# Kernel optimization log

Measured on AMD Instinct MI355X. Metric: run time of the kernel, lower is better.

The kernel has to match this reference:

```python
import jax, jax.numpy as jnp
import numpy as np

TOPK = 13
NUM_CLASSES = 80
ALPHA = 1.0
BETA = 6.0
EPS = 1e-9
DYN_T = 0.4


def _ciou(box1, box2, eps=1e-7):
    # box1, box2: broadcastable [..., 4] in xyxy; returns CIoU [...]
    b1x1, b1y1, b1x2, b1y2 = jnp.split(box1, 4, axis=-1)
    b2x1, b2y1, b2x2, b2y2 = jnp.split(box2, 4, axis=-1)
    w1, h1 = b1x2 - b1x1, b1y2 - b1y1
    w2, h2 = b2x2 - b2x1, b2y2 - b2y1
    inter = (jnp.minimum(b1x2, b2x2) - jnp.maximum(b1x1, b2x1)).clip(0) * \
            (jnp.minimum(b1y2, b2y2) - jnp.maximum(b1y1, b2y1)).clip(0)
    union = w1 * h1 + w2 * h2 - inter + eps
    iou = inter / union
    cw = jnp.maximum(b1x2, b2x2) - jnp.minimum(b1x1, b2x1)   # enclosing box w
    ch = jnp.maximum(b1y2, b2y2) - jnp.minimum(b1y1, b2y1)   # enclosing box h
    c2 = cw ** 2 + ch ** 2 + eps
    rho2 = ((b2x1 + b2x2 - b1x1 - b1x2) ** 2 + (b2y1 + b2y2 - b1y1 - b1y2) ** 2) / 4.0
    v = (4.0 / jnp.pi ** 2) * (jnp.arctan(w2 / h2) - jnp.arctan(w1 / h1)) ** 2
    a = jax.lax.stop_gradient(v / (v - iou + (1.0 + eps)))
    return (iou - (rho2 / c2 + v * a)).squeeze(-1)


def _assign(pd_scores, pd_bboxes, anc_points, gt_labels, gt_bboxes, mask_gt):
    bs, na, nc = pd_scores.shape
    nmax = gt_bboxes.shape[1]
    labels = gt_labels.squeeze(-1)                               # [bs, nmax]

    # --- select_candidates_in_gts: anchor centers inside gt boxes ---
    lt, rb = gt_bboxes[..., :2], gt_bboxes[..., 2:]
    deltas = jnp.concatenate([anc_points[None, None] - lt[:, :, None],
                              rb[:, :, None] - anc_points[None, None]], axis=-1)  # [bs,nmax,na,4]
    mask_in_gts = (deltas.min(-1) > EPS).astype(pd_scores.dtype)  # [bs,nmax,na]

    # --- get_box_metrics ---
    m = (mask_in_gts * mask_gt) > 0                               # [bs,nmax,na] bool
    bb = pd_scores[jnp.arange(bs)[:, None], :, labels]            # [bs,nmax,na]
    bbox_scores = jnp.where(m, bb, 0.0)
    ciou = _ciou(gt_bboxes[:, :, None, :], pd_bboxes[:, None, :, :]).clip(0)
    overlaps = jnp.where(m, ciou, 0.0)                            # [bs,nmax,na]
    align_metric = bbox_scores ** ALPHA * overlaps ** BETA

    # --- select_topk_candidates (count of topk indices; topk_mask unused, as in source) ---
    _, topk_idxs = jax.lax.top_k(align_metric, TOPK)              # [bs,nmax,TOPK]
    b_idx = jnp.arange(bs)[:, None, None]
    n_idx = jnp.arange(nmax)[None, :, None]
    mask_topk = jnp.zeros_like(align_metric).at[b_idx, n_idx, topk_idxs].add(1.0)

    mask_pos = mask_topk * mask_in_gts * mask_gt                  # [bs,nmax,na]

    # --- select_highest_overlaps (unconditional where == torch branch) ---
    fg_mask = mask_pos.sum(-2)                                    # [bs,na]
    mask_multi = (fg_mask[:, None, :] > 1)
    max_idx = overlaps.argmax(1)                                  # [bs,na]
    is_max = (jnp.arange(nmax)[None, :, None] == max_idx[:, None, :]).astype(mask_pos.dtype)
    mask_pos = jnp.where(mask_multi, is_max, mask_pos)
    fg_mask = mask_pos.sum(-2)
    target_gt_idx = mask_pos.argmax(-2)                           # [bs,na]

    # --- get_targets ---
    flat_idx = target_gt_idx + jnp.arange(bs)[:, None] * nmax     # [bs,na]
    target_labels = labels.reshape(-1)[flat_idx]                  # [bs,na]
    target_bboxes = gt_bboxes.reshape(-1, 4)[flat_idx]            # [bs,na,4]
    one_hot = jax.nn.one_hot(target_labels, NUM_CLASSES, dtype=pd_scores.dtype)
    target_scores = jnp.where(fg_mask[..., None] > 0, one_hot, 0.0)  # [bs,na,nc]

    # --- dynamic normalization ---
    align_metric = align_metric * mask_pos
    dynamic_metric = DYN_T * align_metric.max(-1, keepdims=True)  # [bs,nmax,1]
    norm_align = (align_metric / (dynamic_metric + EPS)).max(-2)[..., None]  # [bs,na,1]
    target_scores = target_scores * norm_align

    return target_labels, target_bboxes, target_scores, fg_mask > 0, target_gt_idx


def setup_inputs() -> dict:
    key = jax.random.key(0)
    ks = jax.random.split(key, 6)
    bs, na, nmax, nc = 32, 8400, 64, 80

    def make_boxes(k, shape_prefix):
        k1, k2 = jax.random.split(k)
        c = jax.random.uniform(k1, shape_prefix + (2,), jnp.float32, 0.0, 640.0)
        wh = jax.random.uniform(k2, shape_prefix + (2,), jnp.float32, 8.0, 128.0)
        return jnp.concatenate([c - wh / 2, c + wh / 2], axis=-1)

    return {
        "pd_scores": jax.random.uniform(ks[0], (bs, na, nc), jnp.float32),
        "pd_bboxes": make_boxes(ks[1], (bs, na)),
        "anc_points": jax.random.uniform(ks[2], (na, 2), jnp.float32, 0.0, 640.0),
        "gt_labels": jax.random.randint(ks[3], (bs, nmax, 1), 0, nc),
        "gt_bboxes": make_boxes(ks[4], (bs, nmax)),
        "mask_gt": (jax.random.uniform(ks[5], (bs, nmax, 1)) < 0.9).astype(jnp.float32),
    }


def reference(pd_scores, pd_bboxes, anc_points, gt_labels, gt_bboxes, mask_gt):
    return _assign(pd_scores, pd_bboxes, anc_points, gt_labels, gt_bboxes, mask_gt)
```

## Files before the change

kernel.cpp:

```cpp
#include <hip/hip_runtime.h>
#include <math.h>

#define BS   32
#define NA   8400
#define NMAX 64
#define NC   80
#define TOPKN 13
#define ICAP 1024
#define PCAP 512

#define OFF_LABELS 0
#define OFF_BBOX   (BS*NA)
#define OFF_SCORES (BS*NA + BS*NA*4)
#define OFF_FG     (BS*NA*5 + BS*NA*NC)
#define OFF_TGT    (BS*NA*6 + BS*NA*NC)

__device__ __forceinline__ float ciou_f(float g0, float g1, float g2, float g3,
                                        float p0, float p1, float p2, float p3) {
    const float eps = 1e-7f;
    float w1 = g2 - g0, h1 = g3 - g1;
    float w2 = p2 - p0, h2 = p3 - p1;
    float iw = fmaxf(fminf(g2, p2) - fmaxf(g0, p0), 0.f);
    float ih = fmaxf(fminf(g3, p3) - fmaxf(g1, p1), 0.f);
    float inter = iw * ih;
    float uni = w1 * h1 + w2 * h2 - inter + eps;
    float iou = inter / uni;
    float cw = fmaxf(g2, p2) - fminf(g0, p0);
    float ch = fmaxf(g3, p3) - fminf(g1, p1);
    float c2 = cw * cw + ch * ch + eps;
    float dx = p0 + p2 - g0 - g2;
    float dy = p1 + p3 - g1 - g3;
    float rho2 = (dx * dx + dy * dy) * 0.25f;
    const float four_over_pi2 = 4.0f / 9.869604401089358f;
    float dv = atanf(w2 / h2) - atanf(w1 / h1);
    float v = four_over_pi2 * dv * dv;
    float a = v / (v - iou + (1.0f + eps));
    return iou - (rho2 / c2 + v * a);
}

__device__ __forceinline__ float pow6f(float x) { float x2 = x * x; return x2 * x2 * x2; }

__device__ __forceinline__ float align_at(int a, float g0, float g1, float g2, float g3,
                                          int label, const float* __restrict__ anc,
                                          const float* __restrict__ pb,
                                          const float* __restrict__ ps, float& d_out) {
    float ax = anc[a * 2 + 0], ay = anc[a * 2 + 1];
    float d = fminf(fminf(ax - g0, ay - g1), fminf(g2 - ax, g3 - ay));
    d_out = d;
    float al = 0.f;
    if (d > 1e-9f) {
        float p0 = pb[a * 4 + 0], p1 = pb[a * 4 + 1];
        float p2 = pb[a * 4 + 2], p3 = pb[a * 4 + 3];
        float cv = fmaxf(ciou_f(g0, g1, g2, g3, p0, p1, p2, p3), 0.f);
        if (cv > 0.f) al = ps[a * NC + label] * pow6f(cv);
    }
    return al;
}

__global__ __launch_bounds__(256) void kernA(const float* __restrict__ pd_scores,
                                             const float* __restrict__ pd_bboxes,
                                             const float* __restrict__ anc,
                                             const int*   __restrict__ gt_labels,
                                             const float* __restrict__ gt_bboxes,
                                             const float* __restrict__ mask_gt,
                                             int* __restrict__ claim_count,
                                             int* __restrict__ claimed_j) {
    const int j = blockIdx.x, b = blockIdx.y;
    const int tid = threadIdx.x;
    const int wid = tid >> 6, lane = tid & 63;

    __shared__ int   s_in[ICAP];
    __shared__ float s_pv[PCAP];
    __shared__ int   s_pi[PCAP];
    __shared__ int   s_icnt, s_pcnt;
    __shared__ float s_rv[4];
    __shared__ int   s_ri[4];
    __shared__ int   s_sel[TOPKN];

    if (mask_gt[b * NMAX + j] == 0.f) return;

    if (tid == 0) { s_icnt = 0; s_pcnt = 0; }
    __syncthreads();

    const int   label = gt_labels[b * NMAX + j];
    const float g0 = gt_bboxes[(b * NMAX + j) * 4 + 0];
    const float g1 = gt_bboxes[(b * NMAX + j) * 4 + 1];
    const float g2 = gt_bboxes[(b * NMAX + j) * 4 + 2];
    const float g3 = gt_bboxes[(b * NMAX + j) * 4 + 3];
    const float* pb = pd_bboxes + (size_t)b * NA * 4;
    const float* ps = pd_scores + (size_t)b * NA * NC;
    const float2* anc2 = (const float2*)anc;

    for (int a = tid; a < NA; a += 256) {
        float2 A = anc2[a];
        float d = fminf(fminf(A.x - g0, A.y - g1), fminf(g2 - A.x, g3 - A.y));
        if (d > 1e-9f) {
            int s = atomicAdd(&s_icnt, 1);
            if (s < ICAP) s_in[s] = a;
        }
    }
    __syncthreads();
    const int M = min(s_icnt, ICAP);

    for (int t = tid; t < M; t += 256) {
        int a = s_in[t];
        float p0 = pb[a * 4 + 0], p1 = pb[a * 4 + 1];
        float p2 = pb[a * 4 + 2], p3 = pb[a * 4 + 3];
        float cv = fmaxf(ciou_f(g0, g1, g2, g3, p0, p1, p2, p3), 0.f);
        if (cv > 0.f) {
            float al = ps[a * NC + label] * pow6f(cv);
            int s = atomicAdd(&s_pcnt, 1);
            if (s < PCAP) { s_pv[s] = al; s_pi[s] = a; }
        }
    }
    __syncthreads();
    const int P = min(s_pcnt, PCAP);
    const int K1 = min(P, TOPKN);

    for (int k = 0; k < K1; k++) {
        float bv = -2.f; int bi = NA;
        for (int t = tid; t < P; t += 256) {
            float v = s_pv[t];
            int   i = s_pi[t];
            if (v > bv || (v == bv && i < bi)) { bv = v; bi = i; }
        }
        #pragma unroll
        for (int off = 32; off >= 1; off >>= 1) {
            float v2 = __shfl_down(bv, off, 64);
            int   i2 = __shfl_down(bi, off, 64);
            if (v2 > bv || (v2 == bv && i2 < bi)) { bv = v2; bi = i2; }
        }
        if (lane == 0) { s_rv[wid] = bv; s_ri[wid] = bi; }
        __syncthreads();
        if (tid == 0) {
            float fv = s_rv[0]; int fi = s_ri[0];
            #pragma unroll
            for (int w = 1; w < 4; w++) {
                float v2 = s_rv[w]; int i2 = s_ri[w];
                if (v2 > fv || (v2 == fv && i2 < fi)) { fv = v2; fi = i2; }
            }
            s_sel[k] = fi;
            for (int t = 0; t < P; t++) {
                if (s_pi[t] == fi) { s_pv[t] = -1.f; break; }
            }
        }
        __syncthreads();
    }

    if (tid < K1) {
        int a = s_sel[tid];
        atomicAdd(&claim_count[b * NA + a], 1);
        claimed_j[b * NA + a] = j;
    }

    if (tid == 0 && K1 < TOPKN) {
        int need = TOPKN - K1;
        for (int a = 0; a < NA && need > 0; a++) {
            float d;
            float al = align_at(a, g0, g1, g2, g3, label, anc, pb, ps, d);
            if (al == 0.f) {
                if (d > 1e-9f) {
                    atomicAdd(&claim_count[b * NA + a], 1);
                    claimed_j[b * NA + a] = j;
                }
                need--;
            }
        }
    }
}

__global__ __launch_bounds__(256) void kernB(const float* __restrict__ pd_scores,
                                             const float* __restrict__ pd_bboxes,
                                             const float* __restrict__ anc,
                                             const int*   __restrict__ gt_labels,
                                             const float* __restrict__ gt_bboxes,
                                             const float* __restrict__ mask_gt,
                                             const int* __restrict__ claim_count,
                                             const int* __restrict__ claimed_j,
                                             int* __restrict__ assigned_j,
                                             float* __restrict__ assigned_align,
                                             unsigned int* __restrict__ gt_max,
                                             int* __restrict__ fg_cnt,
                                             int* __restrict__ fg_list,
                                             float* __restrict__ out) {
    int idx = blockIdx.x * blockDim.x + threadIdx.x;
    if (idx >= BS * NA) return;
    int b = idx / NA, a = idx - b * NA;

    int cnt = claim_count[idx];
    int ja = -1;

    if (cnt > 0) {
        float ax = anc[a * 2 + 0], ay = anc[a * 2 + 1];
        float p0 = pd_bboxes[((size_t)b * NA + a) * 4 + 0];
        float p1 = pd_bboxes[((size_t)b * NA + a) * 4 + 1];
        float p2 = pd_bboxes[((size_t)b * NA + a) * 4 + 2];
        float p3 = pd_bboxes[((size_t)b * NA + a) * 4 + 3];

        if (cnt == 1) {
            ja = claimed_j[idx];
        } else {
            float best = -1.f; ja = 0;
            for (int j = 0; j < NMAX; j++) {
                float mgj = mask_gt[b * NMAX + j];
                float ov = 0.f;
                if (mgj != 0.f) {
                    float g0 = gt_bboxes[(b * NMAX + j) * 4 + 0];
                    float g1 = gt_bboxes[(b * NMAX + j) * 4 + 1];
                    float g2 = gt_bboxes[(b * NMAX + j) * 4 + 2];
                    float g3 = gt_bboxes[(b * NMAX + j) * 4 + 3];
                    float d = fminf(fminf(ax - g0, ay - g1), fminf(g2 - ax, g3 - ay));
                    if (d > 1e-9f)
                        ov = fmaxf(ciou_f(g0, g1, g2, g3, p0, p1, p2, p3), 0.f);
                }
                if (ov > best) { best = ov; ja = j; }
            }
        }

        float val = 0.f;
        float mgj = mask_gt[b * NMAX + ja];
        if (mgj != 0.f) {
            float g0 = gt_bboxes[(b * NMAX + ja) * 4 + 0];
            float g1 = gt_bboxes[(b * NMAX + ja) * 4 + 1];
            float g2 = gt_bboxes[(b * NMAX + ja) * 4 + 2];
            float g3 = gt_bboxes[(b * NMAX + ja) * 4 + 3];
            float d = fminf(fminf(ax - g0, ay - g1), fminf(g2 - ax, g3 - ay));
            if (d > 1e-9f) {
                float cv = fmaxf(ciou_f(g0, g1, g2, g3, p0, p1, p2, p3), 0.f);
                if (cv > 0.f) {
                    int lab = gt_labels[b * NMAX + ja];
                    val = pd_scores[((size_t)b * NA + a) * NC + lab] * pow6f(cv);
                }
            }
        }
        assigned_j[idx] = ja;
        assigned_align[idx] = val;
        atomicMax(&gt_max[b * NMAX + ja], __float_as_uint(val));
        int slot = atomicAdd(fg_cnt, 1);
        fg_list[slot] = idx;
    }

    int fg = (cnt > 0);
    int tgt = fg ? ja : 0;
    out[OFF_LABELS + idx] = (float)gt_labels[b * NMAX + tgt];
    const float4 bb = *(const float4*)&gt_bboxes[(b * NMAX + tgt) * 4];
    *(float4*)&out[OFF_BBOX + idx * 4] = bb;
    out[OFF_FG + idx]  = fg ? 1.f : 0.f;
    out[OFF_TGT + idx] = (float)tgt;
}

__global__ __launch_bounds__(256) void kernD(const int* __restrict__ gt_labels,
                                             const int* __restrict__ assigned_j,
                                             const float* __restrict__ assigned_align,
                                             const unsigned int* __restrict__ gt_max,
                                             const int* __restrict__ fg_cnt,
                                             const int* __restrict__ fg_list,
                                             float* __restrict__ out) {
    int t = blockIdx.x * blockDim.x + threadIdx.x;
    if (t >= fg_cnt[0]) return;
    int idx = fg_list[t];
    int b = idx / NA;
    int ja = assigned_j[idx];
    float v = assigned_align[idx];
    float dyn = 0.4f * __uint_as_float(gt_max[b * NMAX + ja]);
    float sc = v / (dyn + 1e-9f);
    int lab = gt_labels[b * NMAX + ja];
    out[OFF_SCORES + (size_t)idx * NC + lab] = sc;
}

extern "C" void kernel_launch(void* const* d_in, const int* in_sizes, int n_in,
                              void* d_out, int out_size, void* d_ws, size_t ws_size,
                              hipStream_t stream) {
    const float* pd_scores = (const float*)d_in[0];
    const float* pd_bboxes = (const float*)d_in[1];
    const float* anc       = (const float*)d_in[2];
    const int*   gt_labels = (const int*)d_in[3];
    const float* gt_bboxes = (const float*)d_in[4];
    const float* mask_gt   = (const float*)d_in[5];
    float* out = (float*)d_out;

    char* ws = (char*)d_ws;
    size_t off = 0;
    int*          claim_count = (int*)(ws + off);          off += (size_t)BS * NA * 4;
    unsigned int* gt_max      = (unsigned int*)(ws + off); off += (size_t)BS * NMAX * 4;
    int*          fg_cnt      = (int*)(ws + off);          off += 16;
    const size_t zero_bytes = off;
    int*          claimed_j      = (int*)(ws + off);       off += (size_t)BS * NA * 4;
    int*          assigned_j     = (int*)(ws + off);       off += (size_t)BS * NA * 4;
    float*        assigned_align = (float*)(ws + off);     off += (size_t)BS * NA * 4;
    int*          fg_list        = (int*)(ws + off);

    hipMemsetAsync(d_ws, 0, zero_bytes, stream);
    hipMemsetAsync(out + OFF_SCORES, 0, (size_t)BS * NA * NC * 4, stream);

    kernA<<<dim3(NMAX, BS), 256, 0, stream>>>(pd_scores, pd_bboxes, anc, gt_labels,
                                              gt_bboxes, mask_gt, claim_count, claimed_j);
    int nanch = BS * NA;
    kernB<<<(nanch + 255) / 256, 256, 0, stream>>>(pd_scores, pd_bboxes, anc, gt_labels,
                                                   gt_bboxes, mask_gt, claim_count, claimed_j,
                                                   assigned_j, assigned_align, gt_max,
                                                   fg_cnt, fg_list, out);
    int maxfg = BS * NMAX * TOPKN;
    kernD<<<(maxfg + 255) / 256, 256, 0, stream>>>(gt_labels, assigned_j, assigned_align,
                                                   gt_max, fg_cnt, fg_list, out);
}
```

Measured before the change: 230.2 us.

## Register-resident top-k selection, drop workspace memset and global fg counter

```diff
diff --git a/kernel.cpp b/kernel.cpp
--- a/kernel.cpp
+++ b/kernel.cpp
@@ -64,7 +64,8 @@
                                              const float* __restrict__ gt_bboxes,
                                              const float* __restrict__ mask_gt,
                                              int* __restrict__ claim_count,
-                                             int* __restrict__ claimed_j) {
+                                             int* __restrict__ claimed_j,
+                                             unsigned int* __restrict__ gt_max) {
     const int j = blockIdx.x, b = blockIdx.y;
     const int tid = threadIdx.x;
     const int wid = tid >> 6, lane = tid & 63;
@@ -75,7 +76,8 @@
     __shared__ int   s_icnt, s_pcnt;
     __shared__ float s_rv[4];
     __shared__ int   s_ri[4];
-    __shared__ int   s_sel[TOPKN];
+
+    if (tid == 0) gt_max[b * NMAX + j] = 0u;
 
     if (mask_gt[b * NMAX + j] == 0.f) return;
 
@@ -115,42 +117,45 @@
     }
     __syncthreads();
     const int P = min(s_pcnt, PCAP);
-    const int K1 = min(P, TOPKN);
-
-    for (int k = 0; k < K1; k++) {
-        float bv = -2.f; int bi = NA;
-        for (int t = tid; t < P; t += 256) {
-            float v = s_pv[t];
-            int   i = s_pi[t];
-            if (v > bv || (v == bv && i < bi)) { bv = v; bi = i; }
-        }
-        #pragma unroll
-        for (int off = 32; off >= 1; off >>= 1) {
-            float v2 = __shfl_down(bv, off, 64);
-            int   i2 = __shfl_down(bi, off, 64);
-            if (v2 > bv || (v2 == bv && i2 < bi)) { bv = v2; bi = i2; }
-        }
-        if (lane == 0) { s_rv[wid] = bv; s_ri[wid] = bi; }
-        __syncthreads();
-        if (tid == 0) {
+    int K1;
+
+    if (P <= TOPKN) {
+        K1 = P;
+        if (tid < P) {
+            int a = s_pi[tid];
+            atomicAdd(&claim_count[b * NA + a], 1);
+            claimed_j[b * NA + a] = j;
+        }
+    } else {
+        K1 = TOPKN;
+        float v0 = -2.f, v1 = -2.f; int i0 = NA, i1 = NA;
+        if (tid < P)       { v0 = s_pv[tid];       i0 = s_pi[tid]; }
+        if (tid + 256 < P) { v1 = s_pv[tid + 256]; i1 = s_pi[tid + 256]; }
+        for (int k = 0; k < TOPKN; k++) {
+            float bv = v0; int bi = i0;
+            if (v1 > bv || (v1 == bv && i1 < bi)) { bv = v1; bi = i1; }
+            #pragma unroll
+            for (int off = 32; off >= 1; off >>= 1) {
+                float v2 = __shfl_down(bv, off, 64);
+                int   i2 = __shfl_down(bi, off, 64);
+                if (v2 > bv || (v2 == bv && i2 < bi)) { bv = v2; bi = i2; }
+            }
+            if (lane == 0) { s_rv[wid] = bv; s_ri[wid] = bi; }
+            __syncthreads();
             float fv = s_rv[0]; int fi = s_ri[0];
             #pragma unroll
             for (int w = 1; w < 4; w++) {
                 float v2 = s_rv[w]; int i2 = s_ri[w];
                 if (v2 > fv || (v2 == fv && i2 < fi)) { fv = v2; fi = i2; }
             }
-            s_sel[k] = fi;
-            for (int t = 0; t < P; t++) {
-                if (s_pi[t] == fi) { s_pv[t] = -1.f; break; }
-            }
-        }
-        __syncthreads();
-    }
-
-    if (tid < K1) {
-        int a = s_sel[tid];
-        atomicAdd(&claim_count[b * NA + a], 1);
-        claimed_j[b * NA + a] = j;
+            if (i0 == fi) v0 = -1.f;
+            if (i1 == fi) v1 = -1.f;
+            if (tid == k) {
+                atomicAdd(&claim_count[b * NA + fi], 1);
+                claimed_j[b * NA + fi] = j;
+            }
+            __syncthreads();
+        }
     }
 
     if (tid == 0 && K1 < TOPKN) {
@@ -175,13 +180,11 @@
                                              const int*   __restrict__ gt_labels,
                                              const float* __restrict__ gt_bboxes,
                                              const float* __restrict__ mask_gt,
-                                             const int* __restrict__ claim_count,
+                                             int* __restrict__ claim_count,
                                              const int* __restrict__ claimed_j,
                                              int* __restrict__ assigned_j,
                                              float* __restrict__ assigned_align,
                                              unsigned int* __restrict__ gt_max,
-                                             int* __restrict__ fg_cnt,
-                                             int* __restrict__ fg_list,
                                              float* __restrict__ out) {
     int idx = blockIdx.x * blockDim.x + threadIdx.x;
     if (idx >= BS * NA) return;
@@ -191,6 +194,8 @@
     int ja = -1;
 
     if (cnt > 0) {
+        claim_count[idx] = 0;
+
         float ax = anc[a * 2 + 0], ay = anc[a * 2 + 1];
         float p0 = pd_bboxes[((size_t)b * NA + a) * 4 + 0];
         float p1 = pd_bboxes[((size_t)b * NA + a) * 4 + 1];
@@ -233,12 +238,10 @@
                 }
             }
         }
-        assigned_j[idx] = ja;
         assigned_align[idx] = val;
         atomicMax(&gt_max[b * NMAX + ja], __float_as_uint(val));
-        int slot = atomicAdd(fg_cnt, 1);
-        fg_list[slot] = idx;
-    }
+    }
+    assigned_j[idx] = ja;
 
     int fg = (cnt > 0);
     int tgt = fg ? ja : 0;
@@ -253,14 +256,12 @@
                                              const int* __restrict__ assigned_j,
                                              const float* __restrict__ assigned_align,
                                              const unsigned int* __restrict__ gt_max,
-                                             const int* __restrict__ fg_cnt,
-                                             const int* __restrict__ fg_list,
                                              float* __restrict__ out) {
-    int t = blockIdx.x * blockDim.x + threadIdx.x;
-    if (t >= fg_cnt[0]) return;
-    int idx = fg_list[t];
+    int idx = blockIdx.x * blockDim.x + threadIdx.x;
+    if (idx >= BS * NA) return;
+    int ja = assigned_j[idx];
+    if (ja < 0) return;
     int b = idx / NA;
-    int ja = assigned_j[idx];
     float v = assigned_align[idx];
     float dyn = 0.4f * __uint_as_float(gt_max[b * NMAX + ja]);
     float sc = v / (dyn + 1e-9f);
@@ -279,28 +280,24 @@
     const float* mask_gt   = (const float*)d_in[5];
     float* out = (float*)d_out;
 
+    int* claim_count = (int*)(out + OFF_SCORES);
+
     char* ws = (char*)d_ws;
     size_t off = 0;
-    int*          claim_count = (int*)(ws + off);          off += (size_t)BS * NA * 4;
-    unsigned int* gt_max      = (unsigned int*)(ws + off); off += (size_t)BS * NMAX * 4;
-    int*          fg_cnt      = (int*)(ws + off);          off += 16;
-    const size_t zero_bytes = off;
     int*          claimed_j      = (int*)(ws + off);       off += (size_t)BS * NA * 4;
     int*          assigned_j     = (int*)(ws + off);       off += (size_t)BS * NA * 4;
     float*        assigned_align = (float*)(ws + off);     off += (size_t)BS * NA * 4;
-    int*          fg_list        = (int*)(ws + off);
-
-    hipMemsetAsync(d_ws, 0, zero_bytes, stream);
+    unsigned int* gt_max         = (unsigned int*)(ws + off);
+
     hipMemsetAsync(out + OFF_SCORES, 0, (size_t)BS * NA * NC * 4, stream);
 
     kernA<<<dim3(NMAX, BS), 256, 0, stream>>>(pd_scores, pd_bboxes, anc, gt_labels,
-                                              gt_bboxes, mask_gt, claim_count, claimed_j);
+                                              gt_bboxes, mask_gt, claim_count, claimed_j,
+                                              gt_max);
     int nanch = BS * NA;
     kernB<<<(nanch + 255) / 256, 256, 0, stream>>>(pd_scores, pd_bboxes, anc, gt_labels,
                                                    gt_bboxes, mask_gt, claim_count, claimed_j,
-                                                   assigned_j, assigned_align, gt_max,
-                                                   fg_cnt, fg_list, out);
-    int maxfg = BS * NMAX * TOPKN;
-    kernD<<<(maxfg + 255) / 256, 256, 0, stream>>>(gt_labels, assigned_j, assigned_align,
-                                                   gt_max, fg_cnt, fg_list, out);
-}
+                                                   assigned_j, assigned_align, gt_max, out);
+    kernD<<<(nanch + 255) / 256, 256, 0, stream>>>(gt_labels, assigned_j, assigned_align,
+                                                   gt_max, out);
+}
```

Measured after the change: 196.4 us. 1.17x faster.
